# Kernel tuning notes

Measured on AMD Instinct MI355X. Metric: run time of the kernel, lower is better.

Reference implementation:

```python
import jax, jax.numpy as jnp
import numpy as np

K = 1024          # num_embeddings
D = 128           # embedding_dim
BETA = 0.25
DECAY = 0.99
EPS = 1e-05
RESTART_THRESHOLD = 0.5


def setup_inputs() -> dict:
    key = jax.random.key(0)
    k1, k2, k3 = jax.random.split(key, 3)
    B, L = 8, 4096
    z_e = jax.random.normal(k1, (B, D, L), dtype=jnp.float32)
    # nn.init.uniform_(embedding, -1/K, 1/K)
    embedding = jax.random.uniform(k2, (K, D), dtype=jnp.float32,
                                   minval=-1.0 / K, maxval=1.0 / K)
    cluster_size = jnp.zeros((K,), dtype=jnp.float32)
    embedding_avg = embedding.copy()
    return {"z_e": z_e, "embedding": embedding,
            "cluster_size": cluster_size, "embedding_avg": embedding_avg}


def reference(z_e, embedding, cluster_size, embedding_avg):
    """Training-mode forward of EMAVectorQuantizer (1D latents, z_e: (B, D, L)).

    Note: in the torch code `e = self.embedding` aliases the buffer, and
    self.embedding.data.copy_(embed_normalized) mutates it in-place BEFORE
    z_q_flat = encodings @ e, so quantization uses the UPDATED codebook.
    We reproduce that ordering here. Random-restart indices use a fixed key.
    """
    B, Dd, L = z_e.shape
    # (B, D, L) -> (B, L, D) -> (N, D)
    z_flat = jnp.transpose(z_e, (0, 2, 1)).reshape(-1, Dd)  # N = B*L
    N = z_flat.shape[0]

    # squared-euclidean distances (N, K) via expansion
    z_sq = jnp.sum(z_flat * z_flat, axis=1, keepdims=True)          # (N, 1)
    e_sq = jnp.sum(embedding * embedding, axis=1)                   # (K,)
    distances = z_sq + e_sq[None, :] - 2.0 * (z_flat @ embedding.T)  # (N, K)
    indices = jnp.argmin(distances, axis=1)                          # (N,)

    # EMA updates (one-hot sums expressed as segment sums)
    counts = jax.ops.segment_sum(jnp.ones((N,), z_flat.dtype), indices, num_segments=K)
    new_cluster = DECAY * cluster_size + (1.0 - DECAY) * counts      # (K,)
    weighted_sum = jax.ops.segment_sum(z_flat, indices, num_segments=K)  # (K, D)
    new_avg = DECAY * embedding_avg + (1.0 - DECAY) * weighted_sum

    # random restart of dead codes (fixed key for determinism)
    dead = new_cluster < RESTART_THRESHOLD                           # (K,) bool
    ridx = jax.random.randint(jax.random.key(42), (K,), 0, N)
    rvec = z_flat[ridx]                                              # (K, D)
    new_cluster = jnp.where(dead, RESTART_THRESHOLD, new_cluster)
    new_avg = jnp.where(dead[:, None], rvec * RESTART_THRESHOLD, new_avg)

    # Laplace-smoothed normalization -> updated codebook
    n = jnp.sum(new_cluster)
    smoothed = (new_cluster + EPS) / (n + K * EPS) * n
    new_embedding = new_avg / smoothed[:, None]                      # (K, D)

    # quantize with the UPDATED codebook (matches torch aliasing semantics)
    z_q_flat = new_embedding[indices]                                # (N, D)
    z_q = jnp.transpose(z_q_flat.reshape(B, L, Dd), (0, 2, 1))       # (B, D, L)

    sg = jax.lax.stop_gradient
    codebook_loss = jnp.mean((sg(z_e) - z_q) ** 2)
    commitment_loss = jnp.mean((z_e - sg(z_q)) ** 2)
    vq_loss = codebook_loss + BETA * commitment_loss

    z_q_st = z_e + sg(z_q - z_e)
    indices_map = indices.reshape(B, L)
    return (z_q_st, indices_map, vq_loss, codebook_loss, BETA * commitment_loss)
```

## Files before the change

### kernel.cpp

```cpp
#include <hip/hip_runtime.h>
#include <stdint.h>

constexpr int BB = 8;
constexpr int LL = 4096;
constexpr int DD = 128;
constexpr int KC = 1024;
constexpr int NN = BB * LL;
constexpr int ZTOT = BB * DD * LL;

#define THREEFRY_PARTITIONABLE 1

typedef float f32x16 __attribute__((ext_vector_type(16)));
typedef short s16x8 __attribute__((ext_vector_type(8)));

union F4S8 { float4 f; s16x8 s; };

__device__ __forceinline__ ushort f2bf(float x) {
  uint32_t u = __float_as_uint(x);
  uint32_t r = u + 0x7FFFu + ((u >> 16) & 1u);
  return (ushort)(r >> 16);
}
__device__ __forceinline__ float bf2f(ushort h) {
  return __uint_as_float(((uint32_t)h) << 16);
}

__device__ __forceinline__ uint32_t rotl32(uint32_t x, int r) {
  return (x << r) | (x >> (32 - r));
}

__device__ __forceinline__ void threefry2x32(uint32_t k0, uint32_t k1,
                                             uint32_t x0, uint32_t x1,
                                             uint32_t* o0, uint32_t* o1) {
  uint32_t ks0 = k0, ks1 = k1, ks2 = 0x1BD11BDAu ^ k0 ^ k1;
  x0 += ks0; x1 += ks1;
  x0 += x1; x1 = rotl32(x1, 13); x1 ^= x0;
  x0 += x1; x1 = rotl32(x1, 15); x1 ^= x0;
  x0 += x1; x1 = rotl32(x1, 26); x1 ^= x0;
  x0 += x1; x1 = rotl32(x1, 6);  x1 ^= x0;
  x0 += ks1; x1 += ks2 + 1u;
  x0 += x1; x1 = rotl32(x1, 17); x1 ^= x0;
  x0 += x1; x1 = rotl32(x1, 29); x1 ^= x0;
  x0 += x1; x1 = rotl32(x1, 16); x1 ^= x0;
  x0 += x1; x1 = rotl32(x1, 24); x1 ^= x0;
  x0 += ks2; x1 += ks0 + 2u;
  x0 += x1; x1 = rotl32(x1, 13); x1 ^= x0;
  x0 += x1; x1 = rotl32(x1, 15); x1 ^= x0;
  x0 += x1; x1 = rotl32(x1, 26); x1 ^= x0;
  x0 += x1; x1 = rotl32(x1, 6);  x1 ^= x0;
  x0 += ks0; x1 += ks1 + 3u;
  x0 += x1; x1 = rotl32(x1, 17); x1 ^= x0;
  x0 += x1; x1 = rotl32(x1, 29); x1 ^= x0;
  x0 += x1; x1 = rotl32(x1, 16); x1 ^= x0;
  x0 += x1; x1 = rotl32(x1, 24); x1 ^= x0;
  x0 += ks1; x1 += ks2 + 4u;
  x0 += x1; x1 = rotl32(x1, 13); x1 ^= x0;
  x0 += x1; x1 = rotl32(x1, 15); x1 ^= x0;
  x0 += x1; x1 = rotl32(x1, 26); x1 ^= x0;
  x0 += x1; x1 = rotl32(x1, 6);  x1 ^= x0;
  x0 += ks2; x1 += ks0 + 5u;
  *o0 = x0; *o1 = x1;
}

__global__ __launch_bounds__(128) void k_prep(const float* __restrict__ E,
                                              float* __restrict__ esq,
                                              double* __restrict__ lacc,
                                              ushort* __restrict__ E0f,
                                              ushort* __restrict__ E1f) {
  const int k = blockIdx.x;
  const int d = threadIdx.x;
  float v = E[k * DD + d];
  __shared__ float r[128];
  __shared__ ushort sh0[128], sh1[128];
  ushort h0 = f2bf(v);
  float v0 = bf2f(h0);
  ushort h1 = f2bf(v - v0);
  sh0[d] = h0; sh1[d] = h1;
  r[d] = v * v;
  __syncthreads();
  for (int s = 64; s > 0; s >>= 1) {
    if (d < s) r[d] += r[d + s];
    __syncthreads();
  }
  if (d == 0) {
    esq[k] = r[0];
    if (k == 0) lacc[0] = 0.0;
  }
  if (d < 32) {
    const ushort* src = (d < 16) ? sh0 : sh1;
    ushort* dst = (d < 16) ? E0f : E1f;
    int p = d & 15, h = p & 1, ks = p >> 1;
    int slot = ((k >> 5) * 8 + ks) * 64 + (k & 31) + 32 * h;
    int off = ks * 16 + h * 8;
    uint32_t w0 = (uint32_t)src[off + 0] | ((uint32_t)src[off + 1] << 16);
    uint32_t w1 = (uint32_t)src[off + 2] | ((uint32_t)src[off + 3] << 16);
    uint32_t w2 = (uint32_t)src[off + 4] | ((uint32_t)src[off + 5] << 16);
    uint32_t w3 = (uint32_t)src[off + 6] | ((uint32_t)src[off + 7] << 16);
    uint4 val; val.x = w0; val.y = w1; val.z = w2; val.w = w3;
    *(uint4*)(dst + (size_t)slot * 8) = val;
  }
}

__global__ __launch_bounds__(256, 4) void k_dist(const float* __restrict__ Z,
                                                 const float* __restrict__ E,
                                                 const ushort* __restrict__ E0f,
                                                 const ushort* __restrict__ E1f,
                                                 const float* __restrict__ esq,
                                                 int* __restrict__ idx_out,
                                                 float* __restrict__ zflat) {
  __shared__ float Zt[128][33];
  __shared__ float esh[1024];
  __shared__ float mv1[4][32], mv2[4][32];
  __shared__ int   mi1[4][32], mi2[4][32];

  const int tid = threadIdx.x;
  const int w = tid >> 6;
  const int lane = tid & 63;
  const int hi = lane >> 5;
  const int rr = lane & 31;
  const int r0 = blockIdx.x * 32;
  const int b = r0 >> 12;
  const int l0 = r0 & (LL - 1);

  const float* zsrc = Z + (size_t)b * DD * LL + l0;
#pragma unroll
  for (int p = 0; p < 4; ++p) {
    int f = p * 256 + tid;
    int d = f >> 3;
    int g = f & 7;
    float4 v = *(const float4*)(zsrc + (size_t)d * LL + g * 4);
    Zt[d][g * 4 + 0] = v.x;
    Zt[d][g * 4 + 1] = v.y;
    Zt[d][g * 4 + 2] = v.z;
    Zt[d][g * 4 + 3] = v.w;
  }
  {
    float4 e4 = *(const float4*)(esq + tid * 4);
    *(float4*)(&esh[tid * 4]) = e4;
  }
  __syncthreads();

  {
    float* dst = zflat + (size_t)r0 * DD;
#pragma unroll
    for (int p = 0; p < 4; ++p) {
      int f = p * 256 + tid;
      int row = f >> 5;
      int dq = f & 31;
      float4 v;
      v.x = Zt[dq * 4 + 0][row];
      v.y = Zt[dq * 4 + 1][row];
      v.z = Zt[dq * 4 + 2][row];
      v.w = Zt[dq * 4 + 3][row];
      *(float4*)(dst + (size_t)row * DD + dq * 4) = v;
    }
  }

  s16x8 B0[8], B1[8];
#pragma unroll
  for (int ks = 0; ks < 8; ++ks) {
    s16x8 b0, b1;
#pragma unroll
    for (int j = 0; j < 8; ++j) {
      float z = Zt[ks * 16 + hi * 8 + j][rr];
      ushort h0 = f2bf(z);
      float z0f = bf2f(h0);
      ushort h1 = f2bf(z - z0f);
      b0[j] = (short)h0;
      b1[j] = (short)h1;
    }
    B0[ks] = b0; B1[ks] = b1;
  }

  float b1v = 3.4e38f, b2v = 3.4e38f;
  int b1i = 0, b2i = 0;
  const float4* e0p = (const float4*)E0f;
  const float4* e1p = (const float4*)E1f;

  for (int s = 0; s < 8; ++s) {
    const int sg = w * 8 + s;
    f32x16 acc;
#pragma unroll
    for (int i = 0; i < 16; ++i) acc[i] = 0.0f;
    const int base = sg * 512 + lane;
#pragma unroll
    for (int ks = 0; ks < 8; ++ks) {
      F4S8 ua, ub;
      ua.f = e0p[base + ks * 64];
      ub.f = e1p[base + ks * 64];
      acc = __builtin_amdgcn_mfma_f32_32x32x16_bf16(ua.s, B0[ks], acc, 0, 0, 0);
      acc = __builtin_amdgcn_mfma_f32_32x32x16_bf16(ua.s, B1[ks], acc, 0, 0, 0);
      acc = __builtin_amdgcn_mfma_f32_32x32x16_bf16(ub.s, B0[ks], acc, 0, 0, 0);
    }
#pragma unroll
    for (int reg = 0; reg < 16; ++reg) {
      int cl = (reg & 3) + 8 * (reg >> 2) + 4 * hi;
      int c = sg * 32 + cl;
      float rv = fmaf(-2.0f, acc[reg], esh[c]);
      if (rv < b1v) { b2v = b1v; b2i = b1i; b1v = rv; b1i = c; }
      else if (rv < b2v) { b2v = rv; b2i = c; }
    }
  }

  float ov1 = __shfl_xor(b1v, 32, 64); int oi1 = __shfl_xor(b1i, 32, 64);
  float ov2 = __shfl_xor(b2v, 32, 64); int oi2 = __shfl_xor(b2i, 32, 64);
  if (ov1 < b1v || (ov1 == b1v && oi1 < b1i)) { b2v = b1v; b2i = b1i; b1v = ov1; b1i = oi1; }
  else if (ov1 < b2v || (ov1 == b2v && oi1 < b2i)) { b2v = ov1; b2i = oi1; }
  if (ov2 < b2v || (ov2 == b2v && oi2 < b2i)) { b2v = ov2; b2i = oi2; }

  if (hi == 0) {
    mv1[w][rr] = b1v; mi1[w][rr] = b1i;
    mv2[w][rr] = b2v; mi2[w][rr] = b2i;
  }
  __syncthreads();

  if (tid < 32) {
    const int row = tid;
    float fb1 = mv1[0][row]; int fi1 = mi1[0][row];
    float fb2 = mv2[0][row]; int fi2 = mi2[0][row];
#pragma unroll
    for (int q = 1; q < 4; ++q) {
      float v1 = mv1[q][row]; int i1 = mi1[q][row];
      float v2 = mv2[q][row]; int i2 = mi2[q][row];
      if (v1 < fb1 || (v1 == fb1 && i1 < fi1)) {
        fb2 = fb1; fi2 = fi1; fb1 = v1; fi1 = i1;
      } else if (v1 < fb2 || (v1 == fb2 && i1 < fi2)) {
        fb2 = v1; fi2 = i1;
      }
      if (v2 < fb2 || (v2 == fb2 && i2 < fi2)) { fb2 = v2; fi2 = i2; }
    }

    int fi = fi1;
    if (fb2 - fb1 <= 4e-5f) {
      float zsq = 0.0f;
#pragma unroll 4
      for (int d = 0; d < 128; ++d) {
        float z = Zt[d][row];
        zsq = fmaf(z, z, zsq);
      }
      float dot1 = 0.0f, dot2 = 0.0f;
      const float* e1r = E + (size_t)fi1 * DD;
      const float* e2r = E + (size_t)fi2 * DD;
      for (int d = 0; d < 128; ++d) {
        float z = Zt[d][row];
        dot1 = fmaf(z, e1r[d], dot1);
        dot2 = fmaf(z, e2r[d], dot2);
      }
      float k1 = (zsq + esh[fi1]) - 2.0f * dot1;
      float k2 = (zsq + esh[fi2]) - 2.0f * dot2;
      if (k2 < k1 || (k2 == k1 && fi2 < fi1)) fi = fi2;
    }
    idx_out[r0 + row] = fi;
  }
}

__global__ __launch_bounds__(1024) void k_hist(const int* __restrict__ idxs,
                                               int* __restrict__ part_cnt) {
  __shared__ int h[1024];
  const int tid = threadIdx.x;
  const int j = blockIdx.x;
  h[tid] = 0;
  __syncthreads();
  int k = idxs[j * 1024 + tid];
  atomicAdd(&h[k], 1);
  __syncthreads();
  part_cnt[j * 1024 + tid] = h[tid];
}

__global__ __launch_bounds__(1024) void k_scan(int* __restrict__ part_cnt,
                                               int* __restrict__ code_start,
                                               int* __restrict__ icnt,
                                               float* __restrict__ counts) {
  const int k = threadIdx.x;
  int base[32];
  int s = 0;
#pragma unroll
  for (int j = 0; j < 32; ++j) {
    base[j] = s;
    s += part_cnt[j * 1024 + k];
  }
  icnt[k] = s;
  counts[k] = (float)s;

  __shared__ int ps[1024];
  ps[k] = s;
  __syncthreads();
  for (int off = 1; off < 1024; off <<= 1) {
    int v = (k >= off) ? ps[k - off] : 0;
    __syncthreads();
    ps[k] += v;
    __syncthreads();
  }
  int excl = ps[k] - s;
  code_start[k] = excl;
#pragma unroll
  for (int j = 0; j < 32; ++j) {
    part_cnt[j * 1024 + k] = excl + base[j];
  }
}

__global__ __launch_bounds__(1024) void k_scatter(const int* __restrict__ idxs,
                                                  const int* __restrict__ part_base,
                                                  int* __restrict__ rowlist) {
  __shared__ int cur[1024];
  const int tid = threadIdx.x;
  const int j = blockIdx.x;
  cur[tid] = part_base[j * 1024 + tid];
  __syncthreads();
  int row = j * 1024 + tid;
  int k = idxs[row];
  int pos = atomicAdd(&cur[k], 1);
  rowlist[pos] = row;
}

__global__ __launch_bounds__(256) void k_wsum2(const float* __restrict__ zflat,
                                               const int* __restrict__ rowlist,
                                               const int* __restrict__ code_start,
                                               const int* __restrict__ icnt,
                                               float* __restrict__ wsum) {
  const int k = blockIdx.x;
  const int tid = threadIdx.x;
  const int h = tid >> 7;
  const int d = tid & 127;
  __shared__ float red[128];

  const int start = code_start[k];
  const int m = icnt[k];
  float acc = 0.0f;
  for (int j = h; j < m; j += 2) {
    int row = rowlist[start + j];
    acc += zflat[(size_t)row * DD + d];
  }
  if (h == 1) red[d] = acc;
  __syncthreads();
  if (h == 0) {
    wsum[k * DD + d] = acc + red[d];
  }
}

__global__ __launch_bounds__(1024) void k_cluster(const float* __restrict__ counts,
                                                  const float* __restrict__ cs_in,
                                                  float* __restrict__ smooth,
                                                  int* __restrict__ ridx,
                                                  int* __restrict__ deadf) {
  const int k = threadIdx.x;
  float c = counts[k];
  float t1 = 0.99f * cs_in[k];
  float t2 = 0.01f * c;
  float nc = t1 + t2;
  bool dead = nc < 0.5f;

  uint32_t bits;
#if THREEFRY_PARTITIONABLE
  {
    uint32_t o0, o1;
    threefry2x32(0u, 42u, 0u, (uint32_t)k, &o0, &o1);
    bits = o0 ^ o1;
  }
#else
  {
    uint32_t o0, o1;
    if (k < 512) { threefry2x32(0u, 42u, (uint32_t)k, (uint32_t)(k + 512), &o0, &o1); bits = o0; }
    else         { threefry2x32(0u, 42u, (uint32_t)(k - 512), (uint32_t)k, &o0, &o1); bits = o1; }
  }
#endif
  int r = (int)(bits & 0x7FFFu);

  float rep = dead ? 0.5f : nc;

  __shared__ float red[1024];
  red[k] = rep;
  __syncthreads();
  for (int s = 512; s > 0; s >>= 1) {
    if (k < s) red[k] += red[k + s];
    __syncthreads();
  }
  float n = red[0];

  float sm = ((rep + 1e-5f) / (n + 0.01024f)) * n;
  smooth[k] = sm;
  ridx[k] = r;
  deadf[k] = dead ? 1 : 0;
}

__global__ __launch_bounds__(256) void k_emb(const float* __restrict__ wsum,
                                             const float* __restrict__ avg_in,
                                             const float* __restrict__ Z,
                                             const float* __restrict__ smooth,
                                             const int* __restrict__ ridx,
                                             const int* __restrict__ deadf,
                                             float* __restrict__ nemb) {
  int kd = blockIdx.x * 256 + threadIdx.x;
  int k = kd >> 7;
  int d = kd & (DD - 1);
  float t1 = 0.99f * avg_in[kd];
  float t2 = 0.01f * wsum[kd];
  float na = t1 + t2;
  if (deadf[k]) {
    int r = ridx[k];
    float zv = Z[((size_t)(r >> 12) * DD + d) * LL + (r & (LL - 1))];
    na = zv * 0.5f;
  }
  nemb[kd] = na / smooth[k];
}

__global__ __launch_bounds__(256) void k_out(const float* __restrict__ Z,
                                             const float* __restrict__ nemb,
                                             const int* __restrict__ idxs,
                                             float* __restrict__ out,
                                             double* __restrict__ lacc) {
  __shared__ float Zt[128][33];
  __shared__ float Ot[128][33];
  __shared__ int sidx[32];
  __shared__ float lred[4];

  const int tid = threadIdx.x;
  const int r0 = blockIdx.x * 32;
  const int b = r0 >> 12;
  const int l0 = r0 & (LL - 1);

  const float* zsrc = Z + (size_t)b * DD * LL + l0;
#pragma unroll
  for (int p = 0; p < 4; ++p) {
    int f = p * 256 + tid;
    int d = f >> 3;
    int g = f & 7;
    float4 v = *(const float4*)(zsrc + (size_t)d * LL + g * 4);
    Zt[d][g * 4 + 0] = v.x;
    Zt[d][g * 4 + 1] = v.y;
    Zt[d][g * 4 + 2] = v.z;
    Zt[d][g * 4 + 3] = v.w;
  }
  if (tid < 32) sidx[tid] = idxs[r0 + tid];
  __syncthreads();

  const int grp = tid >> 5;
  const int ln = tid & 31;
  float lsum = 0.0f;
#pragma unroll
  for (int it = 0; it < 4; ++it) {
    int row = it * 8 + grp;
    int fi = sidx[row];
    float4 q4 = *(const float4*)(nemb + (size_t)fi * DD + ln * 4);
    float z0 = Zt[ln * 4 + 0][row];
    float z1 = Zt[ln * 4 + 1][row];
    float z2 = Zt[ln * 4 + 2][row];
    float z3 = Zt[ln * 4 + 3][row];
    float o0 = z0 + (q4.x - z0);
    float o1 = z1 + (q4.y - z1);
    float o2 = z2 + (q4.z - z2);
    float o3 = z3 + (q4.w - z3);
    Ot[ln * 4 + 0][row] = o0;
    Ot[ln * 4 + 1][row] = o1;
    Ot[ln * 4 + 2][row] = o2;
    Ot[ln * 4 + 3][row] = o3;
    float d0 = z0 - q4.x, d1 = z1 - q4.y, d2 = z2 - q4.z, d3 = z3 - q4.w;
    lsum += d0 * d0 + d1 * d1 + d2 * d2 + d3 * d3;
  }
  __syncthreads();

  float* dstz = out + (size_t)b * DD * LL + l0;
#pragma unroll
  for (int p = 0; p < 4; ++p) {
    int f = p * 256 + tid;
    int d = f >> 3;
    int g = f & 7;
    float4 v;
    v.x = Ot[d][g * 4 + 0];
    v.y = Ot[d][g * 4 + 1];
    v.z = Ot[d][g * 4 + 2];
    v.w = Ot[d][g * 4 + 3];
    *(float4*)(dstz + (size_t)d * LL + g * 4) = v;
  }
  if (tid < 32) out[(size_t)ZTOT + r0 + tid] = (float)sidx[tid];

  for (int off = 32; off > 0; off >>= 1) lsum += __shfl_down(lsum, off, 64);
  if ((tid & 63) == 0) lred[tid >> 6] = lsum;
  __syncthreads();
  if (tid == 0) {
    float tot = (lred[0] + lred[1]) + (lred[2] + lred[3]);
    atomicAdd(lacc, (double)tot);
  }
}

__global__ void k_fin(const double* __restrict__ lacc, float* __restrict__ out) {
  double S = lacc[0];
  float cb = (float)(S / (double)ZTOT);
  float bc = 0.25f * cb;
  float vq = cb + bc;
  float* o = out + (size_t)ZTOT + NN;
  o[0] = vq;
  o[1] = cb;
  o[2] = bc;
}

extern "C" void kernel_launch(void* const* d_in, const int* in_sizes, int n_in,
                              void* d_out, int out_size, void* d_ws, size_t ws_size,
                              hipStream_t stream) {
  const float* Z  = (const float*)d_in[0];
  const float* E  = (const float*)d_in[1];
  const float* CS = (const float*)d_in[2];
  const float* EA = (const float*)d_in[3];
  float* out = (float*)d_out;
  float* ws = (float*)d_ws;

  float* counts = ws;
  float* esq    = ws + 1024;
  float* smooth = ws + 2048;
  int*   ridx   = (int*)(ws + 3072);
  int*   deadf  = (int*)(ws + 4096);
  float* wsum   = ws + 8192;
  float* nemb   = ws + 8192 + 131072;
  int*   idxs   = (int*)(ws + 270336);
  double* lacc  = (double*)(ws + 303104);

  int* rowlist    = (int*)(ws + 303360);
  int* code_start = (int*)(ws + 336128);
  int* icnt       = (int*)(ws + 337152);

  ushort* E0f = (ushort*)nemb;
  ushort* E1f = (ushort*)(nemb + 65536);
  int* part_cnt = (int*)nemb;

  float* zflat = out;

  k_prep<<<KC, DD, 0, stream>>>(E, esq, lacc, E0f, E1f);
  k_dist<<<NN / 32, 256, 0, stream>>>(Z, E, E0f, E1f, esq, idxs, zflat);
  k_hist<<<32, 1024, 0, stream>>>(idxs, part_cnt);
  k_scan<<<1, 1024, 0, stream>>>(part_cnt, code_start, icnt, counts);
  k_scatter<<<32, 1024, 0, stream>>>(idxs, part_cnt, rowlist);
  k_wsum2<<<KC, 256, 0, stream>>>(zflat, rowlist, code_start, icnt, wsum);
  k_cluster<<<1, KC, 0, stream>>>(counts, CS, smooth, ridx, deadf);
  k_emb<<<(KC * DD) / 256, 256, 0, stream>>>(wsum, EA, Z, smooth, ridx, deadf, nemb);
  k_out<<<NN / 32, 256, 0, stream>>>(Z, nemb, idxs, out, lacc);
  k_fin<<<1, 1, 0, stream>>>(lacc, out);
}
```

Baseline: 109.1 us.

## Process 64 rows per distance block and fold cluster/embedding updates into scan and wsum

The distance kernel now handles 64 rows per block with two MFMA accumulators, so each codebook fragment loaded from memory is reused across twice as many rows. The occupancy hint drops to 2 blocks per CU to make room for the extra registers. The cluster-size/restart computation moves into the scan kernel, and the EMA embedding update moves into the weighted-sum kernel. This removes two launches and the round trip of the intermediate weighted sum through global memory. Dead-code restart vectors are now read from the transposed zflat buffer instead of strided Z, at the cost of higher register pressure and fewer resident waves in the distance kernel.

```diff
diff --git a/kernel.cpp b/kernel.cpp
--- a/kernel.cpp
+++ b/kernel.cpp
@@ -100,33 +100,33 @@
   }
 }
 
-__global__ __launch_bounds__(256, 4) void k_dist(const float* __restrict__ Z,
+__global__ __launch_bounds__(256, 2) void k_dist(const float* __restrict__ Z,
                                                  const float* __restrict__ E,
                                                  const ushort* __restrict__ E0f,
                                                  const ushort* __restrict__ E1f,
                                                  const float* __restrict__ esq,
                                                  int* __restrict__ idx_out,
                                                  float* __restrict__ zflat) {
-  __shared__ float Zt[128][33];
+  __shared__ float Zt[128][65];
   __shared__ float esh[1024];
-  __shared__ float mv1[4][32], mv2[4][32];
-  __shared__ int   mi1[4][32], mi2[4][32];
+  __shared__ float mv1[4][64], mv2[4][64];
+  __shared__ int   mi1[4][64], mi2[4][64];
 
   const int tid = threadIdx.x;
   const int w = tid >> 6;
   const int lane = tid & 63;
   const int hi = lane >> 5;
   const int rr = lane & 31;
-  const int r0 = blockIdx.x * 32;
+  const int r0 = blockIdx.x * 64;
   const int b = r0 >> 12;
   const int l0 = r0 & (LL - 1);
 
   const float* zsrc = Z + (size_t)b * DD * LL + l0;
 #pragma unroll
-  for (int p = 0; p < 4; ++p) {
+  for (int p = 0; p < 8; ++p) {
     int f = p * 256 + tid;
-    int d = f >> 3;
-    int g = f & 7;
+    int d = f >> 4;
+    int g = f & 15;
     float4 v = *(const float4*)(zsrc + (size_t)d * LL + g * 4);
     Zt[d][g * 4 + 0] = v.x;
     Zt[d][g * 4 + 1] = v.y;
@@ -142,7 +142,7 @@
   {
     float* dst = zflat + (size_t)r0 * DD;
 #pragma unroll
-    for (int p = 0; p < 4; ++p) {
+    for (int p = 0; p < 8; ++p) {
       int f = p * 256 + tid;
       int row = f >> 5;
       int dq = f & 31;
@@ -155,65 +155,93 @@
     }
   }
 
-  s16x8 B0[8], B1[8];
+  s16x8 B0a[8], B1a[8], B0b[8], B1b[8];
 #pragma unroll
   for (int ks = 0; ks < 8; ++ks) {
-    s16x8 b0, b1;
+    s16x8 b0a, b1a, b0b, b1b;
 #pragma unroll
     for (int j = 0; j < 8; ++j) {
-      float z = Zt[ks * 16 + hi * 8 + j][rr];
-      ushort h0 = f2bf(z);
-      float z0f = bf2f(h0);
-      ushort h1 = f2bf(z - z0f);
-      b0[j] = (short)h0;
-      b1[j] = (short)h1;
-    }
-    B0[ks] = b0; B1[ks] = b1;
-  }
-
-  float b1v = 3.4e38f, b2v = 3.4e38f;
-  int b1i = 0, b2i = 0;
+      int d = ks * 16 + hi * 8 + j;
+      float za = Zt[d][rr];
+      ushort ha0 = f2bf(za);
+      float za0 = bf2f(ha0);
+      ushort ha1 = f2bf(za - za0);
+      b0a[j] = (short)ha0;
+      b1a[j] = (short)ha1;
+      float zb = Zt[d][32 + rr];
+      ushort hb0 = f2bf(zb);
+      float zb0 = bf2f(hb0);
+      ushort hb1 = f2bf(zb - zb0);
+      b0b[j] = (short)hb0;
+      b1b[j] = (short)hb1;
+    }
+    B0a[ks] = b0a; B1a[ks] = b1a;
+    B0b[ks] = b0b; B1b[ks] = b1b;
+  }
+
+  float a1v = 3.4e38f, a2v = 3.4e38f;
+  int a1i = 0, a2i = 0;
+  float c1v = 3.4e38f, c2v = 3.4e38f;
+  int c1i = 0, c2i = 0;
   const float4* e0p = (const float4*)E0f;
   const float4* e1p = (const float4*)E1f;
 
   for (int s = 0; s < 8; ++s) {
     const int sg = w * 8 + s;
-    f32x16 acc;
-#pragma unroll
-    for (int i = 0; i < 16; ++i) acc[i] = 0.0f;
+    f32x16 aa, ac;
+#pragma unroll
+    for (int i = 0; i < 16; ++i) { aa[i] = 0.0f; ac[i] = 0.0f; }
     const int base = sg * 512 + lane;
 #pragma unroll
     for (int ks = 0; ks < 8; ++ks) {
       F4S8 ua, ub;
       ua.f = e0p[base + ks * 64];
       ub.f = e1p[base + ks * 64];
-      acc = __builtin_amdgcn_mfma_f32_32x32x16_bf16(ua.s, B0[ks], acc, 0, 0, 0);
-      acc = __builtin_amdgcn_mfma_f32_32x32x16_bf16(ua.s, B1[ks], acc, 0, 0, 0);
-      acc = __builtin_amdgcn_mfma_f32_32x32x16_bf16(ub.s, B0[ks], acc, 0, 0, 0);
+      aa = __builtin_amdgcn_mfma_f32_32x32x16_bf16(ua.s, B0a[ks], aa, 0, 0, 0);
+      aa = __builtin_amdgcn_mfma_f32_32x32x16_bf16(ua.s, B1a[ks], aa, 0, 0, 0);
+      aa = __builtin_amdgcn_mfma_f32_32x32x16_bf16(ub.s, B0a[ks], aa, 0, 0, 0);
+      ac = __builtin_amdgcn_mfma_f32_32x32x16_bf16(ua.s, B0b[ks], ac, 0, 0, 0);
+      ac = __builtin_amdgcn_mfma_f32_32x32x16_bf16(ua.s, B1b[ks], ac, 0, 0, 0);
+      ac = __builtin_amdgcn_mfma_f32_32x32x16_bf16(ub.s, B0b[ks], ac, 0, 0, 0);
     }
 #pragma unroll
     for (int reg = 0; reg < 16; ++reg) {
       int cl = (reg & 3) + 8 * (reg >> 2) + 4 * hi;
       int c = sg * 32 + cl;
-      float rv = fmaf(-2.0f, acc[reg], esh[c]);
-      if (rv < b1v) { b2v = b1v; b2i = b1i; b1v = rv; b1i = c; }
-      else if (rv < b2v) { b2v = rv; b2i = c; }
-    }
-  }
-
-  float ov1 = __shfl_xor(b1v, 32, 64); int oi1 = __shfl_xor(b1i, 32, 64);
-  float ov2 = __shfl_xor(b2v, 32, 64); int oi2 = __shfl_xor(b2i, 32, 64);
-  if (ov1 < b1v || (ov1 == b1v && oi1 < b1i)) { b2v = b1v; b2i = b1i; b1v = ov1; b1i = oi1; }
-  else if (ov1 < b2v || (ov1 == b2v && oi1 < b2i)) { b2v = ov1; b2i = oi1; }
-  if (ov2 < b2v || (ov2 == b2v && oi2 < b2i)) { b2v = ov2; b2i = oi2; }
+      float eqc = esh[c];
+      float rva = fmaf(-2.0f, aa[reg], eqc);
+      if (rva < a1v) { a2v = a1v; a2i = a1i; a1v = rva; a1i = c; }
+      else if (rva < a2v) { a2v = rva; a2i = c; }
+      float rvc = fmaf(-2.0f, ac[reg], eqc);
+      if (rvc < c1v) { c2v = c1v; c2i = c1i; c1v = rvc; c1i = c; }
+      else if (rvc < c2v) { c2v = rvc; c2i = c; }
+    }
+  }
+
+  {
+    float ov1 = __shfl_xor(a1v, 32, 64); int oi1 = __shfl_xor(a1i, 32, 64);
+    float ov2 = __shfl_xor(a2v, 32, 64); int oi2 = __shfl_xor(a2i, 32, 64);
+    if (ov1 < a1v || (ov1 == a1v && oi1 < a1i)) { a2v = a1v; a2i = a1i; a1v = ov1; a1i = oi1; }
+    else if (ov1 < a2v || (ov1 == a2v && oi1 < a2i)) { a2v = ov1; a2i = oi1; }
+    if (ov2 < a2v || (ov2 == a2v && oi2 < a2i)) { a2v = ov2; a2i = oi2; }
+  }
+  {
+    float ov1 = __shfl_xor(c1v, 32, 64); int oi1 = __shfl_xor(c1i, 32, 64);
+    float ov2 = __shfl_xor(c2v, 32, 64); int oi2 = __shfl_xor(c2i, 32, 64);
+    if (ov1 < c1v || (ov1 == c1v && oi1 < c1i)) { c2v = c1v; c2i = c1i; c1v = ov1; c1i = oi1; }
+    else if (ov1 < c2v || (ov1 == c2v && oi1 < c2i)) { c2v = ov1; c2i = oi1; }
+    if (ov2 < c2v || (ov2 == c2v && oi2 < c2i)) { c2v = ov2; c2i = oi2; }
+  }
 
   if (hi == 0) {
-    mv1[w][rr] = b1v; mi1[w][rr] = b1i;
-    mv2[w][rr] = b2v; mi2[w][rr] = b2i;
-  }
-  __syncthreads();
-
-  if (tid < 32) {
+    mv1[w][rr] = a1v; mi1[w][rr] = a1i;
+    mv2[w][rr] = a2v; mi2[w][rr] = a2i;
+    mv1[w][32 + rr] = c1v; mi1[w][32 + rr] = c1i;
+    mv2[w][32 + rr] = c2v; mi2[w][32 + rr] = c2i;
+  }
+  __syncthreads();
+
+  if (tid < 64) {
     const int row = tid;
     float fb1 = mv1[0][row]; int fi1 = mi1[0][row];
     float fb2 = mv2[0][row]; int fi2 = mi2[0][row];
@@ -269,7 +297,11 @@
 __global__ __launch_bounds__(1024) void k_scan(int* __restrict__ part_cnt,
                                                int* __restrict__ code_start,
                                                int* __restrict__ icnt,
-                                               float* __restrict__ counts) {
+                                               float* __restrict__ counts,
+                                               const float* __restrict__ cs_in,
+                                               float* __restrict__ smooth,
+                                               int* __restrict__ ridx,
+                                               int* __restrict__ deadf) {
   const int k = threadIdx.x;
   int base[32];
   int s = 0;
@@ -296,6 +328,44 @@
   for (int j = 0; j < 32; ++j) {
     part_cnt[j * 1024 + k] = excl + base[j];
   }
+
+  float c = (float)s;
+  float t1 = 0.99f * cs_in[k];
+  float t2 = 0.01f * c;
+  float nc = t1 + t2;
+  bool dead = nc < 0.5f;
+
+  uint32_t bits;
+#if THREEFRY_PARTITIONABLE
+  {
+    uint32_t o0, o1;
+    threefry2x32(0u, 42u, 0u, (uint32_t)k, &o0, &o1);
+    bits = o0 ^ o1;
+  }
+#else
+  {
+    uint32_t o0, o1;
+    if (k < 512) { threefry2x32(0u, 42u, (uint32_t)k, (uint32_t)(k + 512), &o0, &o1); bits = o0; }
+    else         { threefry2x32(0u, 42u, (uint32_t)(k - 512), (uint32_t)k, &o0, &o1); bits = o1; }
+  }
+#endif
+  int r = (int)(bits & 0x7FFFu);
+
+  float rep = dead ? 0.5f : nc;
+
+  __shared__ float fred[1024];
+  fred[k] = rep;
+  __syncthreads();
+  for (int st = 512; st > 0; st >>= 1) {
+    if (k < st) fred[k] += fred[k + st];
+    __syncthreads();
+  }
+  float n = fred[0];
+
+  float sm = ((rep + 1e-5f) / (n + 0.01024f)) * n;
+  smooth[k] = sm;
+  ridx[k] = r;
+  deadf[k] = dead ? 1 : 0;
 }
 
 __global__ __launch_bounds__(1024) void k_scatter(const int* __restrict__ idxs,
@@ -316,7 +386,11 @@
                                                const int* __restrict__ rowlist,
                                                const int* __restrict__ code_start,
                                                const int* __restrict__ icnt,
-                                               float* __restrict__ wsum) {
+                                               const float* __restrict__ avg_in,
+                                               const float* __restrict__ smooth,
+                                               const int* __restrict__ ridx,
+                                               const int* __restrict__ deadf,
+                                               float* __restrict__ nemb) {
   const int k = blockIdx.x;
   const int tid = threadIdx.x;
   const int h = tid >> 7;
@@ -333,74 +407,16 @@
   if (h == 1) red[d] = acc;
   __syncthreads();
   if (h == 0) {
-    wsum[k * DD + d] = acc + red[d];
-  }
-}
-
-__global__ __launch_bounds__(1024) void k_cluster(const float* __restrict__ counts,
-                                                  const float* __restrict__ cs_in,
-                                                  float* __restrict__ smooth,
-                                                  int* __restrict__ ridx,
-                                                  int* __restrict__ deadf) {
-  const int k = threadIdx.x;
-  float c = counts[k];
-  float t1 = 0.99f * cs_in[k];
-  float t2 = 0.01f * c;
-  float nc = t1 + t2;
-  bool dead = nc < 0.5f;
-
-  uint32_t bits;
-#if THREEFRY_PARTITIONABLE
-  {
-    uint32_t o0, o1;
-    threefry2x32(0u, 42u, 0u, (uint32_t)k, &o0, &o1);
-    bits = o0 ^ o1;
-  }
-#else
-  {
-    uint32_t o0, o1;
-    if (k < 512) { threefry2x32(0u, 42u, (uint32_t)k, (uint32_t)(k + 512), &o0, &o1); bits = o0; }
-    else         { threefry2x32(0u, 42u, (uint32_t)(k - 512), (uint32_t)k, &o0, &o1); bits = o1; }
-  }
-#endif
-  int r = (int)(bits & 0x7FFFu);
-
-  float rep = dead ? 0.5f : nc;
-
-  __shared__ float red[1024];
-  red[k] = rep;
-  __syncthreads();
-  for (int s = 512; s > 0; s >>= 1) {
-    if (k < s) red[k] += red[k + s];
-    __syncthreads();
-  }
-  float n = red[0];
-
-  float sm = ((rep + 1e-5f) / (n + 0.01024f)) * n;
-  smooth[k] = sm;
-  ridx[k] = r;
-  deadf[k] = dead ? 1 : 0;
-}
-
-__global__ __launch_bounds__(256) void k_emb(const float* __restrict__ wsum,
-                                             const float* __restrict__ avg_in,
-                                             const float* __restrict__ Z,
-                                             const float* __restrict__ smooth,
-                                             const int* __restrict__ ridx,
-                                             const int* __restrict__ deadf,
-                                             float* __restrict__ nemb) {
-  int kd = blockIdx.x * 256 + threadIdx.x;
-  int k = kd >> 7;
-  int d = kd & (DD - 1);
-  float t1 = 0.99f * avg_in[kd];
-  float t2 = 0.01f * wsum[kd];
-  float na = t1 + t2;
-  if (deadf[k]) {
-    int r = ridx[k];
-    float zv = Z[((size_t)(r >> 12) * DD + d) * LL + (r & (LL - 1))];
-    na = zv * 0.5f;
-  }
-  nemb[kd] = na / smooth[k];
+    float wsumv = acc + red[d];
+    float t1 = 0.99f * avg_in[k * DD + d];
+    float t2 = 0.01f * wsumv;
+    float na = t1 + t2;
+    if (deadf[k]) {
+      int r = ridx[k];
+      na = zflat[(size_t)r * DD + d] * 0.5f;
+    }
+    nemb[k * DD + d] = na / smooth[k];
+  }
 }
 
 __global__ __launch_bounds__(256) void k_out(const float* __restrict__ Z,
@@ -508,7 +524,6 @@
   float* smooth = ws + 2048;
   int*   ridx   = (int*)(ws + 3072);
   int*   deadf  = (int*)(ws + 4096);
-  float* wsum   = ws + 8192;
   float* nemb   = ws + 8192 + 131072;
   int*   idxs   = (int*)(ws + 270336);
   double* lacc  = (double*)(ws + 303104);
@@ -524,13 +539,13 @@
   float* zflat = out;
 
   k_prep<<<KC, DD, 0, stream>>>(E, esq, lacc, E0f, E1f);
-  k_dist<<<NN / 32, 256, 0, stream>>>(Z, E, E0f, E1f, esq, idxs, zflat);
+  k_dist<<<NN / 64, 256, 0, stream>>>(Z, E, E0f, E1f, esq, idxs, zflat);
   k_hist<<<32, 1024, 0, stream>>>(idxs, part_cnt);
-  k_scan<<<1, 1024, 0, stream>>>(part_cnt, code_start, icnt, counts);
+  k_scan<<<1, 1024, 0, stream>>>(part_cnt, code_start, icnt, counts,
+                                 CS, smooth, ridx, deadf);
   k_scatter<<<32, 1024, 0, stream>>>(idxs, part_cnt, rowlist);
-  k_wsum2<<<KC, 256, 0, stream>>>(zflat, rowlist, code_start, icnt, wsum);
-  k_cluster<<<1, KC, 0, stream>>>(counts, CS, smooth, ridx, deadf);
-  k_emb<<<(KC * DD) / 256, 256, 0, stream>>>(wsum, EA, Z, smooth, ridx, deadf, nemb);
+  k_wsum2<<<KC, 256, 0, stream>>>(zflat, rowlist, code_start, icnt,
+                                  EA, smooth, ridx, deadf, nemb);
   k_out<<<NN / 32, 256, 0, stream>>>(Z, nemb, idxs, out, lacc);
   k_fin<<<1, 1, 0, stream>>>(lacc, out);
 }
```

Result: slower. 114.3 us (+4.8%).

## Give each distance wave all codes for its own rows; fuse cluster/emb kernels

Applied to the files above, without the earlier changes.

The distance kernel now loads 128 rows per block, and each wave scans all 1024 codes for its own 32 rows instead of splitting codes across waves. This removes the cross-wave shared-memory top-2 merge and lets each block share codebook fragment loads across four row tiles, kept in step by periodic barriers. The cluster-size/restart logic moves into the scan kernel, and the EMA/normalise step moves into the weighted-sum kernel, removing two launches and the wsum round trip. In exchange the block count drops by four, the Zt tile grows (occupancy hint lowered to 2), and each wave runs a four-times longer serial MFMA loop.

```diff
diff --git a/kernel.cpp b/kernel.cpp
--- a/kernel.cpp
+++ b/kernel.cpp
@@ -100,33 +100,32 @@
   }
 }
 
-__global__ __launch_bounds__(256, 4) void k_dist(const float* __restrict__ Z,
+__global__ __launch_bounds__(256, 2) void k_dist(const float* __restrict__ Z,
                                                  const float* __restrict__ E,
                                                  const ushort* __restrict__ E0f,
                                                  const ushort* __restrict__ E1f,
                                                  const float* __restrict__ esq,
                                                  int* __restrict__ idx_out,
                                                  float* __restrict__ zflat) {
-  __shared__ float Zt[128][33];
+  __shared__ float Zt[128][129];
   __shared__ float esh[1024];
-  __shared__ float mv1[4][32], mv2[4][32];
-  __shared__ int   mi1[4][32], mi2[4][32];
 
   const int tid = threadIdx.x;
   const int w = tid >> 6;
   const int lane = tid & 63;
   const int hi = lane >> 5;
   const int rr = lane & 31;
-  const int r0 = blockIdx.x * 32;
+  const int rloc = w * 32 + rr;
+  const int r0 = blockIdx.x * 128;
   const int b = r0 >> 12;
   const int l0 = r0 & (LL - 1);
 
   const float* zsrc = Z + (size_t)b * DD * LL + l0;
 #pragma unroll
-  for (int p = 0; p < 4; ++p) {
+  for (int p = 0; p < 16; ++p) {
     int f = p * 256 + tid;
-    int d = f >> 3;
-    int g = f & 7;
+    int d = f >> 5;
+    int g = f & 31;
     float4 v = *(const float4*)(zsrc + (size_t)d * LL + g * 4);
     Zt[d][g * 4 + 0] = v.x;
     Zt[d][g * 4 + 1] = v.y;
@@ -142,7 +141,7 @@
   {
     float* dst = zflat + (size_t)r0 * DD;
 #pragma unroll
-    for (int p = 0; p < 4; ++p) {
+    for (int p = 0; p < 16; ++p) {
       int f = p * 256 + tid;
       int row = f >> 5;
       int dq = f & 31;
@@ -161,7 +160,7 @@
     s16x8 b0, b1;
 #pragma unroll
     for (int j = 0; j < 8; ++j) {
-      float z = Zt[ks * 16 + hi * 8 + j][rr];
+      float z = Zt[ks * 16 + hi * 8 + j][rloc];
       ushort h0 = f2bf(z);
       float z0f = bf2f(h0);
       ushort h1 = f2bf(z - z0f);
@@ -176,8 +175,7 @@
   const float4* e0p = (const float4*)E0f;
   const float4* e1p = (const float4*)E1f;
 
-  for (int s = 0; s < 8; ++s) {
-    const int sg = w * 8 + s;
+  for (int sg = 0; sg < 32; ++sg) {
     f32x16 acc;
 #pragma unroll
     for (int i = 0; i < 16; ++i) acc[i] = 0.0f;
@@ -199,6 +197,7 @@
       if (rv < b1v) { b2v = b1v; b2i = b1i; b1v = rv; b1i = c; }
       else if (rv < b2v) { b2v = rv; b2i = c; }
     }
+    if ((sg & 3) == 3) __syncthreads();
   }
 
   float ov1 = __shfl_xor(b1v, 32, 64); int oi1 = __shfl_xor(b1i, 32, 64);
@@ -208,48 +207,27 @@
   if (ov2 < b2v || (ov2 == b2v && oi2 < b2i)) { b2v = ov2; b2i = oi2; }
 
   if (hi == 0) {
-    mv1[w][rr] = b1v; mi1[w][rr] = b1i;
-    mv2[w][rr] = b2v; mi2[w][rr] = b2i;
-  }
-  __syncthreads();
-
-  if (tid < 32) {
-    const int row = tid;
-    float fb1 = mv1[0][row]; int fi1 = mi1[0][row];
-    float fb2 = mv2[0][row]; int fi2 = mi2[0][row];
-#pragma unroll
-    for (int q = 1; q < 4; ++q) {
-      float v1 = mv1[q][row]; int i1 = mi1[q][row];
-      float v2 = mv2[q][row]; int i2 = mi2[q][row];
-      if (v1 < fb1 || (v1 == fb1 && i1 < fi1)) {
-        fb2 = fb1; fi2 = fi1; fb1 = v1; fi1 = i1;
-      } else if (v1 < fb2 || (v1 == fb2 && i1 < fi2)) {
-        fb2 = v1; fi2 = i1;
-      }
-      if (v2 < fb2 || (v2 == fb2 && i2 < fi2)) { fb2 = v2; fi2 = i2; }
-    }
-
-    int fi = fi1;
-    if (fb2 - fb1 <= 4e-5f) {
+    int fi = b1i;
+    if (b2v - b1v <= 4e-5f) {
       float zsq = 0.0f;
 #pragma unroll 4
       for (int d = 0; d < 128; ++d) {
-        float z = Zt[d][row];
+        float z = Zt[d][rloc];
         zsq = fmaf(z, z, zsq);
       }
       float dot1 = 0.0f, dot2 = 0.0f;
-      const float* e1r = E + (size_t)fi1 * DD;
-      const float* e2r = E + (size_t)fi2 * DD;
+      const float* e1r = E + (size_t)b1i * DD;
+      const float* e2r = E + (size_t)b2i * DD;
       for (int d = 0; d < 128; ++d) {
-        float z = Zt[d][row];
+        float z = Zt[d][rloc];
         dot1 = fmaf(z, e1r[d], dot1);
         dot2 = fmaf(z, e2r[d], dot2);
       }
-      float k1 = (zsq + esh[fi1]) - 2.0f * dot1;
-      float k2 = (zsq + esh[fi2]) - 2.0f * dot2;
-      if (k2 < k1 || (k2 == k1 && fi2 < fi1)) fi = fi2;
+      float k1 = (zsq + esh[b1i]) - 2.0f * dot1;
+      float k2 = (zsq + esh[b2i]) - 2.0f * dot2;
+      if (k2 < k1 || (k2 == k1 && b2i < b1i)) fi = b2i;
     }
-    idx_out[r0 + row] = fi;
+    idx_out[r0 + rloc] = fi;
   }
 }
 
@@ -269,7 +247,11 @@
 __global__ __launch_bounds__(1024) void k_scan(int* __restrict__ part_cnt,
                                                int* __restrict__ code_start,
                                                int* __restrict__ icnt,
-                                               float* __restrict__ counts) {
+                                               float* __restrict__ counts,
+                                               const float* __restrict__ cs_in,
+                                               float* __restrict__ smooth,
+                                               int* __restrict__ ridx,
+                                               int* __restrict__ deadf) {
   const int k = threadIdx.x;
   int base[32];
   int s = 0;
@@ -296,6 +278,44 @@
   for (int j = 0; j < 32; ++j) {
     part_cnt[j * 1024 + k] = excl + base[j];
   }
+
+  float c = (float)s;
+  float t1 = 0.99f * cs_in[k];
+  float t2 = 0.01f * c;
+  float nc = t1 + t2;
+  bool dead = nc < 0.5f;
+
+  uint32_t bits;
+#if THREEFRY_PARTITIONABLE
+  {
+    uint32_t o0, o1;
+    threefry2x32(0u, 42u, 0u, (uint32_t)k, &o0, &o1);
+    bits = o0 ^ o1;
+  }
+#else
+  {
+    uint32_t o0, o1;
+    if (k < 512) { threefry2x32(0u, 42u, (uint32_t)k, (uint32_t)(k + 512), &o0, &o1); bits = o0; }
+    else         { threefry2x32(0u, 42u, (uint32_t)(k - 512), (uint32_t)k, &o0, &o1); bits = o1; }
+  }
+#endif
+  int r = (int)(bits & 0x7FFFu);
+
+  float rep = dead ? 0.5f : nc;
+
+  __shared__ float fred[1024];
+  fred[k] = rep;
+  __syncthreads();
+  for (int st = 512; st > 0; st >>= 1) {
+    if (k < st) fred[k] += fred[k + st];
+    __syncthreads();
+  }
+  float n = fred[0];
+
+  float sm = ((rep + 1e-5f) / (n + 0.01024f)) * n;
+  smooth[k] = sm;
+  ridx[k] = r;
+  deadf[k] = dead ? 1 : 0;
 }
 
 __global__ __launch_bounds__(1024) void k_scatter(const int* __restrict__ idxs,
@@ -316,7 +336,11 @@
                                                const int* __restrict__ rowlist,
                                                const int* __restrict__ code_start,
                                                const int* __restrict__ icnt,
-                                               float* __restrict__ wsum) {
+                                               const float* __restrict__ avg_in,
+                                               const float* __restrict__ smooth,
+                                               const int* __restrict__ ridx,
+                                               const int* __restrict__ deadf,
+                                               float* __restrict__ nemb) {
   const int k = blockIdx.x;
   const int tid = threadIdx.x;
   const int h = tid >> 7;
@@ -333,74 +357,16 @@
   if (h == 1) red[d] = acc;
   __syncthreads();
   if (h == 0) {
-    wsum[k * DD + d] = acc + red[d];
-  }
-}
-
-__global__ __launch_bounds__(1024) void k_cluster(const float* __restrict__ counts,
-                                                  const float* __restrict__ cs_in,
-                                                  float* __restrict__ smooth,
-                                                  int* __restrict__ ridx,
-                                                  int* __restrict__ deadf) {
-  const int k = threadIdx.x;
-  float c = counts[k];
-  float t1 = 0.99f * cs_in[k];
-  float t2 = 0.01f * c;
-  float nc = t1 + t2;
-  bool dead = nc < 0.5f;
-
-  uint32_t bits;
-#if THREEFRY_PARTITIONABLE
-  {
-    uint32_t o0, o1;
-    threefry2x32(0u, 42u, 0u, (uint32_t)k, &o0, &o1);
-    bits = o0 ^ o1;
-  }
-#else
-  {
-    uint32_t o0, o1;
-    if (k < 512) { threefry2x32(0u, 42u, (uint32_t)k, (uint32_t)(k + 512), &o0, &o1); bits = o0; }
-    else         { threefry2x32(0u, 42u, (uint32_t)(k - 512), (uint32_t)k, &o0, &o1); bits = o1; }
-  }
-#endif
-  int r = (int)(bits & 0x7FFFu);
-
-  float rep = dead ? 0.5f : nc;
-
-  __shared__ float red[1024];
-  red[k] = rep;
-  __syncthreads();
-  for (int s = 512; s > 0; s >>= 1) {
-    if (k < s) red[k] += red[k + s];
-    __syncthreads();
-  }
-  float n = red[0];
-
-  float sm = ((rep + 1e-5f) / (n + 0.01024f)) * n;
-  smooth[k] = sm;
-  ridx[k] = r;
-  deadf[k] = dead ? 1 : 0;
-}
-
-__global__ __launch_bounds__(256) void k_emb(const float* __restrict__ wsum,
-                                             const float* __restrict__ avg_in,
-                                             const float* __restrict__ Z,
-                                             const float* __restrict__ smooth,
-                                             const int* __restrict__ ridx,
-                                             const int* __restrict__ deadf,
-                                             float* __restrict__ nemb) {
-  int kd = blockIdx.x * 256 + threadIdx.x;
-  int k = kd >> 7;
-  int d = kd & (DD - 1);
-  float t1 = 0.99f * avg_in[kd];
-  float t2 = 0.01f * wsum[kd];
-  float na = t1 + t2;
-  if (deadf[k]) {
-    int r = ridx[k];
-    float zv = Z[((size_t)(r >> 12) * DD + d) * LL + (r & (LL - 1))];
-    na = zv * 0.5f;
-  }
-  nemb[kd] = na / smooth[k];
+    float wsumv = acc + red[d];
+    float t1 = 0.99f * avg_in[k * DD + d];
+    float t2 = 0.01f * wsumv;
+    float na = t1 + t2;
+    if (deadf[k]) {
+      int r = ridx[k];
+      na = zflat[(size_t)r * DD + d] * 0.5f;
+    }
+    nemb[k * DD + d] = na / smooth[k];
+  }
 }
 
 __global__ __launch_bounds__(256) void k_out(const float* __restrict__ Z,
@@ -508,7 +474,6 @@
   float* smooth = ws + 2048;
   int*   ridx   = (int*)(ws + 3072);
   int*   deadf  = (int*)(ws + 4096);
-  float* wsum   = ws + 8192;
   float* nemb   = ws + 8192 + 131072;
   int*   idxs   = (int*)(ws + 270336);
   double* lacc  = (double*)(ws + 303104);
@@ -524,13 +489,13 @@
   float* zflat = out;
 
   k_prep<<<KC, DD, 0, stream>>>(E, esq, lacc, E0f, E1f);
-  k_dist<<<NN / 32, 256, 0, stream>>>(Z, E, E0f, E1f, esq, idxs, zflat);
+  k_dist<<<NN / 128, 256, 0, stream>>>(Z, E, E0f, E1f, esq, idxs, zflat);
   k_hist<<<32, 1024, 0, stream>>>(idxs, part_cnt);
-  k_scan<<<1, 1024, 0, stream>>>(part_cnt, code_start, icnt, counts);
+  k_scan<<<1, 1024, 0, stream>>>(part_cnt, code_start, icnt, counts,
+                                 CS, smooth, ridx, deadf);
   k_scatter<<<32, 1024, 0, stream>>>(idxs, part_cnt, rowlist);
-  k_wsum2<<<KC, 256, 0, stream>>>(zflat, rowlist, code_start, icnt, wsum);
-  k_cluster<<<1, KC, 0, stream>>>(counts, CS, smooth, ridx, deadf);
-  k_emb<<<(KC * DD) / 256, 256, 0, stream>>>(wsum, EA, Z, smooth, ridx, deadf, nemb);
+  k_wsum2<<<KC, 256, 0, stream>>>(zflat, rowlist, code_start, icnt,
+                                  EA, smooth, ridx, deadf, nemb);
   k_out<<<NN / 32, 256, 0, stream>>>(Z, nemb, idxs, out, lacc);
   k_fin<<<1, 1, 0, stream>>>(lacc, out);
 }
```

Measured after the change: 179.8 us. 1.65x slower.
